# Performance work log

Hardware: AMD Instinct MI355X
Metric: run time of the kernel (lower is better)

Reference implementation:

```python
import jax, jax.numpy as jnp
import numpy as np

B, S, H = 2, 2048, 2048
NH, NG = 16, 4           # attention heads, query groups
HD = H // NH             # head_dim = 128
HPG = NH // NG           # heads per group = 4


def setup_inputs() -> dict:
    key = jax.random.key(0)
    ks = jax.random.split(key, 8)
    s = 0.02
    return {
        "hidden_states": jax.random.normal(ks[0], (B, S, H), dtype=jnp.float32),
        "attention_mask": jnp.ones((B, S), dtype=jnp.int32),
        "Wq": jax.random.normal(ks[1], (H, H), dtype=jnp.float32) * s,
        "bq": jnp.zeros((H,), dtype=jnp.float32),
        "Wk": jax.random.normal(ks[2], (HD * NG, H), dtype=jnp.float32) * s,
        "bk": jnp.zeros((HD * NG,), dtype=jnp.float32),
        "Wv": jax.random.normal(ks[3], (HD * NG, H), dtype=jnp.float32) * s,
        "bv": jnp.zeros((HD * NG,), dtype=jnp.float32),
    }


def reference(hidden_states, attention_mask, Wq, bq, Wk, bk, Wv, bv):
    b, s, _ = hidden_states.shape
    scale = 1.0 / np.sqrt(HD).astype(np.float32)
    # projections (torch Linear: x @ W.T + b)
    q = hidden_states @ Wq.T + bq                      # [b,s,H]
    k = hidden_states @ Wk.T + bk                      # [b,s,NG*HD]
    v = hidden_states @ Wv.T + bv
    # q grouped so that repeat_interleave of k/v along heads == broadcast over heads_per_group
    q = q.reshape(b, s, NG, HPG, HD)                   # heads = group-major order
    k = k.reshape(b, s, NG, HD)
    v = v.reshape(b, s, NG, HD)
    scores = jnp.einsum("bsgpd,btgd->bgpst", q, k) * scale  # [b,NG,HPG,s,s]
    # mask: positions with attention_mask == 0 get finfo.min added
    mask_add = jnp.where(attention_mask == 0,
                         jnp.finfo(scores.dtype).min,
                         jnp.float32(0.0))             # [b,t]
    scores = scores + mask_add[:, None, None, None, :]
    attn = jax.nn.softmax(scores, axis=-1)             # dropout is identity in eval
    out = jnp.einsum("bgpst,btgd->bsgpd", attn, v)     # [b,s,NG,HPG,HD]
    return out.reshape(b, s, NH * HD)
```

## Files before the change

kernel.cpp:

```cpp
#include <hip/hip_runtime.h>
#include <hip/hip_bf16.h>

#define B_ 2
#define S_ 2048
#define H_ 2048
#define NH_ 16
#define NG_ 4
#define HD_ 128
#define HPG_ 4

typedef __attribute__((ext_vector_type(8))) short short8;
typedef __attribute__((ext_vector_type(4))) short short4v;
typedef __attribute__((ext_vector_type(4))) float float4v;

#define MFMA_BF16 __builtin_amdgcn_mfma_f32_16x16x32_bf16

#if __has_builtin(__builtin_amdgcn_exp2f)
#define EXP2(x) __builtin_amdgcn_exp2f(x)
#else
#define EXP2(x) exp2f(x)
#endif

__device__ __forceinline__ void gload16(const void* g, void* l) {
    __builtin_amdgcn_global_load_lds(
        (const __attribute__((address_space(1))) unsigned int*)g,
        (__attribute__((address_space(3))) unsigned int*)l, 16, 0, 0);
}

__device__ __forceinline__ short bf16bits(float f) {
    union { __hip_bfloat16 h; short s; } u;
    u.h = __float2bfloat16(f);
    return u.s;
}

__global__ __launch_bounds__(256) void cvt_all(const float* __restrict__ hs,
                                               const float* __restrict__ wq,
                                               const float* __restrict__ wk,
                                               const float* __restrict__ wv,
                                               const int* __restrict__ mask,
                                               const float* __restrict__ bq,
                                               const float* __restrict__ bk,
                                               const float* __restrict__ bv,
                                               __hip_bfloat16* __restrict__ o_hs,
                                               __hip_bfloat16* __restrict__ o_wq,
                                               __hip_bfloat16* __restrict__ o_wk,
                                               __hip_bfloat16* __restrict__ o_wv,
                                               float* __restrict__ o_m,
                                               float* __restrict__ o_bc) {
    int i = blockIdx.x * 256 + threadIdx.x;
    if (blockIdx.x == 0) {
#pragma unroll
        for (int j = 0; j < 16; ++j) {
            int idx = threadIdx.x * 16 + j;
            o_m[idx] = mask[idx] ? 0.0f : -3.0e38f;
        }
    }
    if (blockIdx.x == 1) {
#pragma unroll
        for (int j = 0; j < 12; ++j) {
            int idx = j * 256 + threadIdx.x;
            float v = (idx < 2048) ? bq[idx] : (idx < 2560) ? bk[idx - 2048] : bv[idx - 2560];
            o_bc[idx] = v;
        }
    }
    const float* src;
    __hip_bfloat16* dst;
    int off;
    if (i < 1048576)      { src = hs; dst = o_hs; off = i; }
    else if (i < 1572864) { src = wq; dst = o_wq; off = i - 1048576; }
    else if (i < 1703936) { src = wk; dst = o_wk; off = i - 1572864; }
    else                  { src = wv; dst = o_wv; off = i - 1703936; }
    const float4* s4 = (const float4*)src;
    float4 a = s4[2 * (size_t)off];
    float4 b = s4[2 * (size_t)off + 1];
    union { short8 s; __hip_bfloat16 h[8]; } u;
    u.h[0] = __float2bfloat16(a.x); u.h[1] = __float2bfloat16(a.y);
    u.h[2] = __float2bfloat16(a.z); u.h[3] = __float2bfloat16(a.w);
    u.h[4] = __float2bfloat16(b.x); u.h[5] = __float2bfloat16(b.y);
    u.h[6] = __float2bfloat16(b.z); u.h[7] = __float2bfloat16(b.w);
    *(short8*)(dst + 8 * (size_t)off) = u.s;
}

__global__ __launch_bounds__(512, 2) void gemm_qkv3(const __hip_bfloat16* __restrict__ A,
                                                    const __hip_bfloat16* __restrict__ Wcat,
                                                    const float* __restrict__ biasC,
                                                    __hip_bfloat16* __restrict__ qO,
                                                    __hip_bfloat16* __restrict__ kO,
                                                    __hip_bfloat16* __restrict__ vTO) {
    extern __shared__ char lds[];

    const int tid = threadIdx.x;
    const int lane = tid & 63;
    const int x = lane & 15, g = lane >> 4;
    const int wid = tid >> 6;
    const int wm = wid >> 2, wn = wid & 3;

    const int id0 = blockIdx.x;
    const int id = ((id0 & 7) << 5) | (id0 >> 3);
    const int bn_t = id >> 4, bm_t = id & 15;
    const int bm = bm_t * 256, bn = bn_t * 192;
    const int K = 2048;

    const int srow = tid >> 2;
    const int schunk = (tid & 3) ^ ((tid >> 3) & 3);
    const __hip_bfloat16* gA0 = A + (size_t)(bm + srow) * K + schunk * 8;
    const __hip_bfloat16* gA1 = A + (size_t)(bm + 128 + srow) * K + schunk * 8;
    const __hip_bfloat16* gB0 = Wcat + (size_t)(bn + srow) * K + schunk * 8;
    const __hip_bfloat16* gB1 = Wcat + (size_t)(bn + 128 + srow) * K + schunk * 8;
    const bool doB1 = (tid < 256);

    const int xk = (x >> 1) & 3;
    int aoffA[8], boffB[3];
#pragma unroll
    for (int mb = 0; mb < 8; ++mb)
        aoffA[mb] = (wm * 128 + mb * 16 + x) * 64 + ((g ^ xk) * 16);
#pragma unroll
    for (int nb = 0; nb < 3; ++nb)
        boffB[nb] = 16384 + (wn * 48 + nb * 16 + x) * 64 + ((g ^ xk) * 16);

    float4v acc[8][3];
#pragma unroll
    for (int i = 0; i < 8; ++i)
#pragma unroll
        for (int j = 0; j < 3; ++j) acc[i][j] = (float4v)0.f;

#pragma unroll
    for (int p = 0; p < 2; ++p) {
        char* stg = lds + p * 28672;
        gload16(gA0, stg + tid * 16);
        gload16(gA1, stg + 8192 + tid * 16);
        gload16(gB0, stg + 16384 + tid * 16);
        if (doB1) gload16(gB1, stg + 24576 + tid * 16);
        gA0 += 32; gA1 += 32; gB0 += 32; gB1 += 32;
    }
    if (doB1) asm volatile("s_waitcnt vmcnt(4)" ::: "memory");
    else      asm volatile("s_waitcnt vmcnt(3)" ::: "memory");
    __builtin_amdgcn_s_barrier();

#pragma unroll 4
    for (int t = 0; t < 64; ++t) {
        const char* bc = lds + (t & 3) * 28672;
        char* stg = lds + ((t + 2) & 3) * 28672;

        short8 afA[4], bfr[3];
#pragma unroll
        for (int mb = 0; mb < 4; ++mb) afA[mb] = *(const short8*)(bc + aoffA[mb]);
#pragma unroll
        for (int nb = 0; nb < 3; ++nb) bfr[nb] = *(const short8*)(bc + boffB[nb]);
        if (t < 62) {
            gload16(gA0, stg + tid * 16);
            gload16(gA1, stg + 8192 + tid * 16);
            gA0 += 32; gA1 += 32;
        }
        __builtin_amdgcn_s_barrier();
        asm volatile("s_waitcnt lgkmcnt(0)");
        __builtin_amdgcn_sched_barrier(0);
        __builtin_amdgcn_s_setprio(1);
#pragma unroll
        for (int mb = 0; mb < 4; ++mb)
#pragma unroll
            for (int nb = 0; nb < 3; ++nb)
                acc[mb][nb] = MFMA_BF16(afA[mb], bfr[nb], acc[mb][nb], 0, 0, 0);
        __builtin_amdgcn_s_setprio(0);
        __builtin_amdgcn_s_barrier();

        short8 afB[4];
#pragma unroll
        for (int mb = 0; mb < 4; ++mb) afB[mb] = *(const short8*)(bc + aoffA[4 + mb]);
        if (t < 62) {
            gload16(gB0, stg + 16384 + tid * 16);
            if (doB1) gload16(gB1, stg + 24576 + tid * 16);
            gB0 += 32; gB1 += 32;
        }
        __builtin_amdgcn_s_barrier();
        asm volatile("s_waitcnt lgkmcnt(0)");
        __builtin_amdgcn_sched_barrier(0);
        __builtin_amdgcn_s_setprio(1);
#pragma unroll
        for (int mb = 0; mb < 4; ++mb)
#pragma unroll
            for (int nb = 0; nb < 3; ++nb)
                acc[4 + mb][nb] = MFMA_BF16(afB[mb], bfr[nb], acc[4 + mb][nb], 0, 0, 0);
        __builtin_amdgcn_s_setprio(0);
        if (t < 62) {
            if (doB1) asm volatile("s_waitcnt vmcnt(4)" ::: "memory");
            else      asm volatile("s_waitcnt vmcnt(3)" ::: "memory");
        } else {
            asm volatile("s_waitcnt vmcnt(0)" ::: "memory");
        }
        __builtin_amdgcn_s_barrier();
    }

#pragma unroll
    for (int mb = 0; mb < 8; ++mb) {
#pragma unroll
        for (int nb = 0; nb < 3; ++nb) {
            const int n = bn + wn * 48 + nb * 16 + x;
            const float bsv = biasC[n];
            const int m0 = bm + wm * 128 + mb * 16 + g * 4;
            if (n < 2048) {
#pragma unroll
                for (int r = 0; r < 4; ++r)
                    qO[(size_t)(m0 + r) * 2048 + n] = __float2bfloat16(acc[mb][nb][r] + bsv);
            } else if (n < 2560) {
                const int nk = n - 2048;
#pragma unroll
                for (int r = 0; r < 4; ++r)
                    kO[(size_t)(m0 + r) * 512 + nk] = __float2bfloat16(acc[mb][nb][r] + bsv);
            } else {
                const int nv = n - 2560;
                const int gv = nv >> 7, d = nv & 127;
                const int bb2 = m0 >> 11, s = m0 & 2047;
                short4v pk;
#pragma unroll
                for (int r = 0; r < 4; ++r) pk[r] = bf16bits(acc[mb][nb][r] + bsv);
                *(short4v*)(vTO + ((size_t)(bb2 * NG_ + gv) * HD_ + d) * S_ + s) = pk;
            }
        }
    }
}

__global__ __launch_bounds__(512, 2) void attn(const __hip_bfloat16* __restrict__ q,
                                               const __hip_bfloat16* __restrict__ k,
                                               const __hip_bfloat16* __restrict__ vT,
                                               const float* __restrict__ M,
                                               float* __restrict__ out) {
    extern __shared__ char smem[];
    char* Ks = smem;
    char* Vs = smem + 32768;
    char* Ps = smem + 49152;

    const int tid = threadIdx.x;
    const int lane = tid & 63;
    const int w = tid >> 6;
    const int wm = w >> 2, wn = w & 3;
    const int x = lane & 15, g = lane >> 4;

    const int bid0 = blockIdx.x;
    const int bid = ((bid0 & 7) << 5) | (bid0 >> 3);
    const int qt = bid & 7;
    const int hp = (bid >> 3) & 3;
    const int gi = (bid >> 5) & 3;
    const int b = bid >> 7;
    const int head = gi * HPG_ + hp;
    const int q0 = qt * 256;

    short8 qf[4][4];
#pragma unroll
    for (int nb = 0; nb < 4; ++nb) {
        const int qq = q0 + wn * 64 + nb * 16 + x;
        const __hip_bfloat16* qrow = q + ((size_t)(b * S_ + qq) * NH_ + head) * HD_ + g * 8;
#pragma unroll
        for (int ks = 0; ks < 4; ++ks)
            qf[nb][ks] = *(const short8*)(qrow + ks * 32);
    }

    const int kchunk = (tid & 15) ^ ((tid >> 4) & 15);
    const __hip_bfloat16* kp = k + ((size_t)(b * S_ + (tid >> 4)) * NG_ + gi) * HD_ + kchunk * 8;
    const int vchunk = (tid & 7) ^ ((tid >> 3) & 7);
    const __hip_bfloat16* vp = vT + ((size_t)(b * NG_ + gi) * HD_ + (tid >> 3)) * S_ + vchunk * 8;
    const float* mp = M + b * S_ + wm * 32 + g * 4;

    float4v O[4][4];
#pragma unroll
    for (int i = 0; i < 4; ++i)
#pragma unroll
        for (int j = 0; j < 4; ++j) O[i][j] = (float4v)0.f;
    float l_part[4] = {0.f, 0.f, 0.f, 0.f};

    const float SM = 0.08838834764831845f * 1.4426950408889634f;

    gload16(kp, Ks + tid * 16);
    gload16(kp + 16384, Ks + tid * 16 + 8192);
    kp += 32768;

    for (int it = 0; it < 32; ++it) {
        __syncthreads();
        const int p = it & 1;
        const char* KsC = Ks + p * 16384;

        float4 mv0 = *(const float4*)(mp);
        float4 mv1 = *(const float4*)(mp + 16);
        mp += 64;
        gload16(vp, Vs + tid * 16);
        gload16(vp + 131072, Vs + tid * 16 + 8192);
        vp += 64;
        if (it < 31) {
            char* KsN = Ks + (p ^ 1) * 16384;
            gload16(kp, KsN + tid * 16);
            gload16(kp + 16384, KsN + tid * 16 + 8192);
            kp += 32768;
        }

        float4v sc[2][4];
#pragma unroll
        for (int i = 0; i < 2; ++i)
#pragma unroll
            for (int j = 0; j < 4; ++j) sc[i][j] = (float4v)0.f;
        __builtin_amdgcn_s_setprio(1);
#pragma unroll
        for (int ks = 0; ks < 4; ++ks) {
            short8 af0 = *(const short8*)(KsC + (wm * 32 + x) * 256 + (((ks * 4 + g) ^ x) * 16));
            short8 af1 = *(const short8*)(KsC + (wm * 32 + 16 + x) * 256 + (((ks * 4 + g) ^ x) * 16));
#pragma unroll
            for (int nb = 0; nb < 4; ++nb) {
                sc[0][nb] = MFMA_BF16(af0, qf[nb][ks], sc[0][nb], 0, 0, 0);
                sc[1][nb] = MFMA_BF16(af1, qf[nb][ks], sc[1][nb], 0, 0, 0);
            }
        }
        __builtin_amdgcn_s_setprio(0);

#pragma unroll
        for (int mb = 0; mb < 2; ++mb) {
            const float4 mv = mb ? mv1 : mv0;
            const int hs = wm * 8 + mb * 4 + g;
#pragma unroll
            for (int nb = 0; nb < 4; ++nb) {
                float p0 = EXP2(fmaf(sc[mb][nb][0], SM, mv.x));
                float p1 = EXP2(fmaf(sc[mb][nb][1], SM, mv.y));
                float p2 = EXP2(fmaf(sc[mb][nb][2], SM, mv.z));
                float p3 = EXP2(fmaf(sc[mb][nb][3], SM, mv.w));
                l_part[nb] += (p0 + p1) + (p2 + p3);
                short4v pk;
                pk[0] = bf16bits(p0); pk[1] = bf16bits(p1);
                pk[2] = bf16bits(p2); pk[3] = bf16bits(p3);
                *(short4v*)(Ps + (wn * 64 + nb * 16 + x) * 136 + hs * 8) = pk;
            }
        }

        __syncthreads();

#pragma unroll
        for (int ks = 0; ks < 2; ++ks) {
            short8 vf[4], pf[4];
#pragma unroll
            for (int i4 = 0; i4 < 4; ++i4) {
                vf[i4] = *(const short8*)(Vs + (wm * 64 + i4 * 16 + x) * 128 +
                                          (((ks * 4 + g) ^ (x & 7)) * 16));
                const char* pb = Ps + (wn * 64 + i4 * 16 + x) * 136 + (8 * ks + 2 * g) * 8;
                union { short4v h[2]; short8 s8; } uu;
                uu.h[0] = *(const short4v*)pb;
                uu.h[1] = *(const short4v*)(pb + 8);
                pf[i4] = uu.s8;
            }
            __builtin_amdgcn_s_setprio(1);
#pragma unroll
            for (int mb = 0; mb < 4; ++mb)
#pragma unroll
                for (int nb = 0; nb < 4; ++nb)
                    O[mb][nb] = MFMA_BF16(vf[mb], pf[nb], O[mb][nb], 0, 0, 0);
            __builtin_amdgcn_s_setprio(0);
        }
    }

    __syncthreads();
#pragma unroll
    for (int nb = 0; nb < 4; ++nb) {
        l_part[nb] += __shfl_xor(l_part[nb], 16);
        l_part[nb] += __shfl_xor(l_part[nb], 32);
    }
    float* lws = (float*)Ps;
    if (g == 0) {
#pragma unroll
        for (int nb = 0; nb < 4; ++nb)
            lws[wm * 256 + wn * 64 + nb * 16 + x] = l_part[nb];
    }
    __syncthreads();
    float inv[4];
#pragma unroll
    for (int nb = 0; nb < 4; ++nb)
        inv[nb] = 1.0f / (l_part[nb] + lws[(wm ^ 1) * 256 + wn * 64 + nb * 16 + x]);

#pragma unroll
    for (int mb = 0; mb < 4; ++mb) {
#pragma unroll
        for (int nb = 0; nb < 4; ++nb) {
            const int qq = q0 + wn * 64 + nb * 16 + x;
            const int d0 = wm * 64 + mb * 16 + g * 4;
            float4v o = O[mb][nb] * inv[nb];
            *(float4v*)(out + (size_t)(b * S_ + qq) * H_ + head * HD_ + d0) = o;
        }
    }
}

extern "C" void kernel_launch(void* const* d_in, const int* in_sizes, int n_in,
                              void* d_out, int out_size, void* d_ws, size_t ws_size,
                              hipStream_t stream) {
    (void)in_sizes; (void)n_in; (void)out_size; (void)ws_size;
    const float* hs = (const float*)d_in[0];
    const int* amask = (const int*)d_in[1];
    const float* Wq = (const float*)d_in[2];
    const float* bq = (const float*)d_in[3];
    const float* Wk = (const float*)d_in[4];
    const float* bk = (const float*)d_in[5];
    const float* Wv = (const float*)d_in[6];
    const float* bv = (const float*)d_in[7];
    float* out = (float*)d_out;

    char* ws = (char*)d_ws;
    __hip_bfloat16* hsB = (__hip_bfloat16*)(ws);
    __hip_bfloat16* WqB = (__hip_bfloat16*)(ws + 16777216);
    __hip_bfloat16* WkB = (__hip_bfloat16*)(ws + 25165824);
    __hip_bfloat16* WvB = (__hip_bfloat16*)(ws + 27262976);
    __hip_bfloat16* qB  = (__hip_bfloat16*)(ws + 29360128);
    __hip_bfloat16* kB  = (__hip_bfloat16*)(ws + 46137344);
    __hip_bfloat16* vTB = (__hip_bfloat16*)(ws + 50331648);
    float* Mf           = (float*)(ws + 54525952);
    float* biasC        = (float*)(ws + 54542336);

    hipFuncSetAttribute((const void*)gemm_qkv3,
                        hipFuncAttributeMaxDynamicSharedMemorySize, 114688);
    hipFuncSetAttribute((const void*)attn,
                        hipFuncAttributeMaxDynamicSharedMemorySize, 83968);

    cvt_all<<<7168, 256, 0, stream>>>(hs, Wq, Wk, Wv, amask, bq, bk, bv,
                                      hsB, WqB, WkB, WvB, Mf, biasC);
    gemm_qkv3<<<256, 512, 114688, stream>>>(hsB, WqB, biasC, qB, kB, vTB);
    attn<<<256, 512, 83968, stream>>>(qB, kB, vTB, Mf, out);
}
```

Before: 231.2 us.

## Restructure QKV GEMM to double-buffered BK=64 tiles with single barrier

Replaces the 4-stage, BK=32 ping-pong pipeline with two split A/B load phases by a simple double buffer of BK=64 tiles. Each iteration issues the next tile's global-to-LDS loads, then runs two k-substeps of MFMAs on the current tile. It waits on vmcnt(0) with one barrier per iteration, using an 8-chunk XOR swizzle. This halves the iteration count and barrier overhead, but loses the fine-grained interleaving and deeper prefetch. LDS use also grows to about 112KB, which may limit occupancy to one block per CU.

```diff
diff --git a/kernel.cpp b/kernel.cpp
--- a/kernel.cpp
+++ b/kernel.cpp
@@ -99,24 +99,23 @@
     const int id = ((id0 & 7) << 5) | (id0 >> 3);
     const int bn_t = id >> 4, bm_t = id & 15;
     const int bm = bm_t * 256, bn = bn_t * 192;
-    const int K = 2048;
-
-    const int srow = tid >> 2;
-    const int schunk = (tid & 3) ^ ((tid >> 3) & 3);
-    const __hip_bfloat16* gA0 = A + (size_t)(bm + srow) * K + schunk * 8;
-    const __hip_bfloat16* gA1 = A + (size_t)(bm + 128 + srow) * K + schunk * 8;
-    const __hip_bfloat16* gB0 = Wcat + (size_t)(bn + srow) * K + schunk * 8;
-    const __hip_bfloat16* gB1 = Wcat + (size_t)(bn + 128 + srow) * K + schunk * 8;
-    const bool doB1 = (tid < 256);
-
-    const int xk = (x >> 1) & 3;
-    int aoffA[8], boffB[3];
+
+    const int srow = tid >> 3;
+    const int schunk = (tid & 7) ^ (srow & 7);
+    const __hip_bfloat16* gA = A + (size_t)(bm + srow) * 2048 + schunk * 8;
+    const __hip_bfloat16* gB = Wcat + (size_t)(bn + srow) * 2048 + schunk * 8;
+
+    int aoff[8][2], boff[3][2];
 #pragma unroll
     for (int mb = 0; mb < 8; ++mb)
-        aoffA[mb] = (wm * 128 + mb * 16 + x) * 64 + ((g ^ xk) * 16);
+#pragma unroll
+        for (int kk = 0; kk < 2; ++kk)
+            aoff[mb][kk] = (wm * 128 + mb * 16 + x) * 128 + (((kk * 4 + g) ^ (x & 7)) * 16);
 #pragma unroll
     for (int nb = 0; nb < 3; ++nb)
-        boffB[nb] = 16384 + (wn * 48 + nb * 16 + x) * 64 + ((g ^ xk) * 16);
+#pragma unroll
+        for (int kk = 0; kk < 2; ++kk)
+            boff[nb][kk] = 32768 + (wn * 48 + nb * 16 + x) * 128 + (((kk * 4 + g) ^ (x & 7)) * 16);
 
     float4v acc[8][3];
 #pragma unroll
@@ -125,69 +124,46 @@
         for (int j = 0; j < 3; ++j) acc[i][j] = (float4v)0.f;
 
 #pragma unroll
-    for (int p = 0; p < 2; ++p) {
-        char* stg = lds + p * 28672;
-        gload16(gA0, stg + tid * 16);
-        gload16(gA1, stg + 8192 + tid * 16);
-        gload16(gB0, stg + 16384 + tid * 16);
-        if (doB1) gload16(gB1, stg + 24576 + tid * 16);
-        gA0 += 32; gA1 += 32; gB0 += 32; gB1 += 32;
-    }
-    if (doB1) asm volatile("s_waitcnt vmcnt(4)" ::: "memory");
-    else      asm volatile("s_waitcnt vmcnt(3)" ::: "memory");
+    for (int p = 0; p < 4; ++p)
+        gload16(gA + (size_t)p * 131072, lds + p * 8192 + tid * 16);
+#pragma unroll
+    for (int p = 0; p < 3; ++p)
+        gload16(gB + (size_t)p * 131072, lds + 32768 + p * 8192 + tid * 16);
+    gA += 64; gB += 64;
+    asm volatile("s_waitcnt vmcnt(0)" ::: "memory");
     __builtin_amdgcn_s_barrier();
 
-#pragma unroll 4
-    for (int t = 0; t < 64; ++t) {
-        const char* bc = lds + (t & 3) * 28672;
-        char* stg = lds + ((t + 2) & 3) * 28672;
-
-        short8 afA[4], bfr[3];
-#pragma unroll
-        for (int mb = 0; mb < 4; ++mb) afA[mb] = *(const short8*)(bc + aoffA[mb]);
-#pragma unroll
-        for (int nb = 0; nb < 3; ++nb) bfr[nb] = *(const short8*)(bc + boffB[nb]);
-        if (t < 62) {
-            gload16(gA0, stg + tid * 16);
-            gload16(gA1, stg + 8192 + tid * 16);
-            gA0 += 32; gA1 += 32;
-        }
-        __builtin_amdgcn_s_barrier();
-        asm volatile("s_waitcnt lgkmcnt(0)");
-        __builtin_amdgcn_sched_barrier(0);
-        __builtin_amdgcn_s_setprio(1);
-#pragma unroll
-        for (int mb = 0; mb < 4; ++mb)
-#pragma unroll
-            for (int nb = 0; nb < 3; ++nb)
-                acc[mb][nb] = MFMA_BF16(afA[mb], bfr[nb], acc[mb][nb], 0, 0, 0);
-        __builtin_amdgcn_s_setprio(0);
-        __builtin_amdgcn_s_barrier();
-
-        short8 afB[4];
-#pragma unroll
-        for (int mb = 0; mb < 4; ++mb) afB[mb] = *(const short8*)(bc + aoffA[4 + mb]);
-        if (t < 62) {
-            gload16(gB0, stg + 16384 + tid * 16);
-            if (doB1) gload16(gB1, stg + 24576 + tid * 16);
-            gB0 += 32; gB1 += 32;
-        }
-        __builtin_amdgcn_s_barrier();
-        asm volatile("s_waitcnt lgkmcnt(0)");
-        __builtin_amdgcn_sched_barrier(0);
-        __builtin_amdgcn_s_setprio(1);
-#pragma unroll
-        for (int mb = 0; mb < 4; ++mb)
-#pragma unroll
-            for (int nb = 0; nb < 3; ++nb)
-                acc[4 + mb][nb] = MFMA_BF16(afB[mb], bfr[nb], acc[4 + mb][nb], 0, 0, 0);
-        __builtin_amdgcn_s_setprio(0);
-        if (t < 62) {
-            if (doB1) asm volatile("s_waitcnt vmcnt(4)" ::: "memory");
-            else      asm volatile("s_waitcnt vmcnt(3)" ::: "memory");
-        } else {
-            asm volatile("s_waitcnt vmcnt(0)" ::: "memory");
-        }
+    for (int t = 0; t < 32; ++t) {
+        const char* cur = lds + (t & 1) * 57344;
+        char* nxt = lds + ((t & 1) ^ 1) * 57344;
+
+        if (t < 31) {
+#pragma unroll
+            for (int p = 0; p < 4; ++p)
+                gload16(gA + (size_t)p * 131072, nxt + p * 8192 + tid * 16);
+#pragma unroll
+            for (int p = 0; p < 3; ++p)
+                gload16(gB + (size_t)p * 131072, nxt + 32768 + p * 8192 + tid * 16);
+            gA += 64; gB += 64;
+        }
+
+#pragma unroll
+        for (int kk = 0; kk < 2; ++kk) {
+            short8 af[8], bf[3];
+#pragma unroll
+            for (int mb = 0; mb < 8; ++mb) af[mb] = *(const short8*)(cur + aoff[mb][kk]);
+#pragma unroll
+            for (int nb = 0; nb < 3; ++nb) bf[nb] = *(const short8*)(cur + boff[nb][kk]);
+            __builtin_amdgcn_s_setprio(1);
+#pragma unroll
+            for (int mb = 0; mb < 8; ++mb)
+#pragma unroll
+                for (int nb = 0; nb < 3; ++nb)
+                    acc[mb][nb] = MFMA_BF16(af[mb], bf[nb], acc[mb][nb], 0, 0, 0);
+            __builtin_amdgcn_s_setprio(0);
+        }
+
+        asm volatile("s_waitcnt vmcnt(0)" ::: "memory");
         __builtin_amdgcn_s_barrier();
     }
 
```

After: 227.0 us (median of 3 runs). About the same (-1.8%).
